# Kernel tuning notes

Measured on AMD Instinct MI355X. Metric: run time of the kernel, lower is better.

## Reference

```python
import jax, jax.numpy as jnp
import numpy as np

B, N, C_IN, C_OUT, K, D_EMB = 32, 4096, 64, 64, 2, 16


def setup_inputs() -> dict:
    key = jax.random.key(0)
    ks = jax.random.split(key, 7)
    x = jax.random.normal(ks[0], (B, N, C_IN), jnp.float32)
    node_embeddings = jax.random.normal(ks[1], (N, D_EMB), jnp.float32)
    weights_pool = jax.random.normal(ks[2], (D_EMB, K, C_IN, C_OUT), jnp.float32) * 0.1
    bias_pool = jax.random.normal(ks[3], (D_EMB, C_OUT), jnp.float32) * 0.1
    lin_w = jax.random.normal(ks[4], (C_OUT, C_IN), jnp.float32) * 0.1
    lin_b = jax.random.normal(ks[5], (C_OUT,), jnp.float32) * 0.1
    adj = jax.random.uniform(ks[6], (N, N), jnp.float32)
    return dict(x=x, node_embeddings=node_embeddings, weights_pool=weights_pool,
                bias_pool=bias_pool, lin_w=lin_w, lin_b=lin_b, adj=adj)


def _sym_norm_adj(W):
    # W + 0.5*I, then D^{-1/2} W D^{-1/2} with D = diag(rowsum)
    n = W.shape[0]
    W = W + 0.5 * jnp.eye(n, dtype=W.dtype)
    sd = jnp.sqrt(1.0 / jnp.sum(W, axis=1))
    return sd[:, None] * W * sd[None, :]


def reference(x, node_embeddings, weights_pool, bias_pool, lin_w, lin_b, adj):
    n = node_embeddings.shape[0]
    # adaptive adjacency: softmax(relu(E E^T)) over neighbors
    supports_dyn = jax.nn.softmax(jax.nn.relu(node_embeddings @ node_embeddings.T), axis=1)
    supports = jnp.stack([jnp.eye(n, dtype=x.dtype), supports_dyn], axis=0)  # [K=2, N, N]
    # node-adaptive weights/bias generated from embeddings
    weights = jnp.einsum('nd,dkio->nkio', node_embeddings, weights_pool)  # [N,K,Cin,Cout]
    bias = node_embeddings @ bias_pool  # [N, Cout]
    # multi-hop aggregation + per-node conv
    x_g = jnp.einsum('knm,bmc->bnkc', supports, x)  # [B,N,K,Cin]
    x_gconv = jnp.einsum('bnki,nkio->bno', x_g, weights) + bias[None]  # [B,N,Cout]
    # static branch: init applies F.softmax(dim=1) to sym-normed adj, forward re-softmaxes dim=-1
    A = jax.nn.softmax(jax.nn.softmax(_sym_norm_adj(adj), axis=1), axis=-1)
    # einsum 'nm,bmc->bmc' == scale node m by sum_n A[n,m]
    scale = jnp.sum(A, axis=0)  # [N]
    x_static = (scale[None, :, None] * x) @ lin_w.T + lin_b  # [B,N,Cout]
    return x_gconv + jax.nn.sigmoid(x_static) * x_static
```

## Files before the change

### kernel.cpp

```cpp
#include <hip/hip_runtime.h>
#include <stdint.h>

#define Bdim 32
#define Ndim 4096
#define Cin  64
#define Cout 64
#define Demb 16

typedef __bf16 bf16x8 __attribute__((ext_vector_type(8)));
typedef float  f32x4  __attribute__((ext_vector_type(4)));

#define GLOBAL_AS(p) ((__attribute__((address_space(1))) void*)(p))
#define LDS_AS(p)    ((__attribute__((address_space(3))) void*)(p))

__device__ __forceinline__ uint16_t f2bf(float x) {
    union { float f; uint32_t u; } v; v.f = x;
    uint32_t r = v.u + 0x7FFFu + ((v.u >> 16) & 1u);
    return (uint16_t)(r >> 16);
}

__device__ __forceinline__ bf16x8 pack8(float4 a, float4 b) {
    union { uint16_t u[8]; bf16x8 v; } r;
    r.u[0] = f2bf(a.x); r.u[1] = f2bf(a.y); r.u[2] = f2bf(a.z); r.u[3] = f2bf(a.w);
    r.u[4] = f2bf(b.x); r.u[5] = f2bf(b.y); r.u[6] = f2bf(b.z); r.u[7] = f2bf(b.w);
    return r.v;
}

__global__ __launch_bounds__(256) void p1_prep(const float* __restrict__ E,
                                               const float* __restrict__ x,
                                               const float* __restrict__ adj,
                                               const float* __restrict__ pool,
                                               uint16_t* __restrict__ A,
                                               float* __restrict__ invA,
                                               uint16_t* __restrict__ Xtt,
                                               float* __restrict__ sd,
                                               float* __restrict__ scale,
                                               float* __restrict__ poolT) {
    __shared__ __align__(16) uint8_t smem[9232];
    const int t = threadIdx.x;
    const int blk = blockIdx.x;

    if (blk < 256) {
        float* Er_s = (float*)smem;
        float* red_s = (float*)(smem + 1024);
        const int n0 = blk * 16;
        Er_s[t] = E[n0 * Demb + t];
        __syncthreads();
        for (int half = 0; half < 2; ++half) {
            float er[8][16];
#pragma unroll
            for (int r = 0; r < 8; ++r)
#pragma unroll
                for (int d = 0; d < 16; ++d) er[r][d] = Er_s[(half * 8 + r) * 16 + d];
            float sacc[8];
#pragma unroll
            for (int r = 0; r < 8; ++r) sacc[r] = 0.f;
            for (int c = 0; c < 16; ++c) {
                const int m = c * 256 + t;
                const float4* ep = (const float4*)(E + (size_t)m * Demb);
                float4 e0 = ep[0], e1 = ep[1], e2 = ep[2], e3 = ep[3];
                float em[16] = {e0.x, e0.y, e0.z, e0.w, e1.x, e1.y, e1.z, e1.w,
                                e2.x, e2.y, e2.z, e2.w, e3.x, e3.y, e3.z, e3.w};
#pragma unroll
                for (int r = 0; r < 8; ++r) {
                    float v = 0.f;
#pragma unroll
                    for (int d = 0; d < 16; ++d) v = fmaf(er[r][d], em[d], v);
                    v = fmaxf(v, 0.f);
                    const float e = __expf(v);
                    sacc[r] += e;
                    A[(size_t)(n0 + half * 8 + r) * Ndim + m] = f2bf(e);
                }
            }
#pragma unroll
            for (int r = 0; r < 8; ++r) {
                float s = sacc[r];
#pragma unroll
                for (int off = 32; off > 0; off >>= 1) s += __shfl_down(s, off, 64);
                __syncthreads();
                if ((t & 63) == 0) red_s[t >> 6] = s;
                __syncthreads();
                if (t == 0)
                    invA[n0 + half * 8 + r] = 1.f / (red_s[0] + red_s[1] + red_s[2] + red_s[3]);
            }
            __syncthreads();
        }
    } else if (blk < 2304) {
        auto T = (uint16_t(*)[72])smem;
        const int idx = blk - 256;
        const int m0 = (idx & 63) * 64;
        const int b = idx >> 6;
        const int c = t & 63;
#pragma unroll
        for (int j = 0; j < 16; ++j) {
            const int m = (t >> 6) + j * 4;
            T[c][m] = f2bf(x[((size_t)b * Ndim + (m0 + m)) * Cin + c]);
        }
        __syncthreads();
        const int c2 = t >> 2, mo = (t & 3) * 16;
        const uint4* src = (const uint4*)&T[c2][mo];
        uint4 v0 = src[0], v1 = src[1];
        uint4* dst = (uint4*)(Xtt + (size_t)(b * Cin + c2) * Ndim + m0 + mo);
        dst[0] = v0;
        dst[1] = v1;
    } else if (blk < 6400) {
        float* red_s = (float*)smem;
        const int n = blk - 2304;
        if (n < 16) scale[n * 256 + t] = 0.f;
        const float4* ap = (const float4*)(adj + (size_t)n * Ndim);
        float s = 0.f;
#pragma unroll
        for (int q = 0; q < 4; ++q) {
            float4 a = ap[q * 256 + t];
            s += a.x + a.y + a.z + a.w;
        }
#pragma unroll
        for (int off = 32; off > 0; off >>= 1) s += __shfl_down(s, off, 64);
        if ((t & 63) == 0) red_s[t >> 6] = s;
        __syncthreads();
        if (t == 0) sd[n] = sqrtf(1.f / (red_s[0] + red_s[1] + red_s[2] + red_s[3] + 0.5f));
    } else {
        const int idx = blk - 6400;
        const int d = idx >> 2;
        const int base = (idx & 3) * 2048;
#pragma unroll
        for (int j = 0; j < 8; ++j) {
            const int e = base + j * 256 + t;
            const float v = pool[d * 8192 + e];
            poolT[d * 8192 + (e & 63) * 128 + (e >> 6)] = v;
        }
    }
}

__global__ __launch_bounds__(256) void p2_mid(const float* __restrict__ E,
                                              const float* __restrict__ adj,
                                              const float* __restrict__ sd,
                                              const float* __restrict__ poolT,
                                              const float* __restrict__ bias_pool,
                                              float* __restrict__ scale,
                                              uint16_t* __restrict__ Wt,
                                              float* __restrict__ biasn) {
    __shared__ __align__(16) uint8_t smem[16384];
    const int t = threadIdx.x;
    const int blk = blockIdx.x;

    if (blk < 256) {
        float* cs = (float*)smem;
#pragma unroll
        for (int i = 0; i < 16; ++i) cs[i * 256 + t] = 0.f;
        __syncthreads();

        const int wv = t >> 6, l = t & 63;
        const int nb = blk * 16 + wv * 4;

        float sdm[64];
#pragma unroll
        for (int i = 0; i < 16; ++i) {
            float4 s4 = *(const float4*)(sd + i * 256 + l * 4);
            sdm[i * 4 + 0] = s4.x; sdm[i * 4 + 1] = s4.y;
            sdm[i * 4 + 2] = s4.z; sdm[i * 4 + 3] = s4.w;
        }
        float colsum[64];
#pragma unroll
        for (int k = 0; k < 64; ++k) colsum[k] = 0.f;

        for (int r = 0; r < 4; ++r) {
            const int n = nb + r;
            const float sdn = sd[n];
            float e1[64];
            float s1 = 0.f;
#pragma unroll
            for (int i = 0; i < 16; ++i) {
                float4 a4 = *(const float4*)(adj + (size_t)n * Ndim + i * 256 + l * 4);
                const int c0 = i * 256 + l * 4;
                float vv[4] = {a4.x, a4.y, a4.z, a4.w};
#pragma unroll
                for (int u = 0; u < 4; ++u) {
                    const float vd = vv[u] + ((c0 + u) == n ? 0.5f : 0.f);
                    const float e = __expf(sdn * vd * sdm[i * 4 + u]);
                    e1[i * 4 + u] = e;
                    s1 += e;
                }
            }
#pragma unroll
            for (int off = 32; off > 0; off >>= 1) s1 += __shfl_xor(s1, off, 64);
            const float inv1 = 1.f / s1;
            float s2 = 0.f;
#pragma unroll
            for (int k = 0; k < 64; ++k) {
                const float e = __expf(e1[k] * inv1);
                e1[k] = e;
                s2 += e;
            }
#pragma unroll
            for (int off = 32; off > 0; off >>= 1) s2 += __shfl_xor(s2, off, 64);
            const float inv2 = 1.f / s2;
#pragma unroll
            for (int k = 0; k < 64; ++k) colsum[k] = fmaf(e1[k], inv2, colsum[k]);
        }
#pragma unroll
        for (int k = 0; k < 64; ++k)
            atomicAdd(&cs[(k >> 2) * 256 + l * 4 + (k & 3)], colsum[k]);
        __syncthreads();
#pragma unroll
        for (int i = 0; i < 16; ++i)
            atomicAdd(scale + i * 256 + t, cs[i * 256 + t]);
    } else {
        float* En = (float*)smem;
        const int idx = blk - 256;
        const int ec = idx & 7;
        const int n0 = (idx >> 3) * 32;
        En[t] = E[n0 * Demb + t];
        En[t + 256] = E[n0 * Demb + t + 256];
        __syncthreads();

        const int e0 = ec * 1024 + t * 4;
        float4 P[16];
#pragma unroll
        for (int d = 0; d < 16; ++d) P[d] = *(const float4*)(poolT + d * 8192 + e0);

        for (int g = 0; g < 32; ++g) {
            float4 acc = {0.f, 0.f, 0.f, 0.f};
#pragma unroll
            for (int d = 0; d < 16; ++d) {
                const float e = En[g * 16 + d];
                acc.x = fmaf(e, P[d].x, acc.x);
                acc.y = fmaf(e, P[d].y, acc.y);
                acc.z = fmaf(e, P[d].z, acc.z);
                acc.w = fmaf(e, P[d].w, acc.w);
            }
            union { uint16_t u[4]; uint2 v; } r;
            r.u[0] = f2bf(acc.x); r.u[1] = f2bf(acc.y);
            r.u[2] = f2bf(acc.z); r.u[3] = f2bf(acc.w);
            *(uint2*)(Wt + (size_t)(n0 + g) * 8192 + e0) = r.v;
        }

        if (ec == 0) {
            const int o = t & 63, gq = t >> 6;
#pragma unroll
            for (int gi = 0; gi < 8; ++gi) {
                const int g = gi * 4 + gq;
                float a = 0.f;
#pragma unroll
                for (int d = 0; d < 16; ++d) a = fmaf(En[g * 16 + d], bias_pool[d * 64 + o], a);
                biasn[(size_t)(n0 + g) * 64 + o] = a;
            }
        }
    }
}

#define GK 4096
#define GN 2048
__global__ __launch_bounds__(256) void k3_gemm(const uint16_t* __restrict__ Abf,
                                               const uint16_t* __restrict__ Bbf,
                                               const float* __restrict__ invA,
                                               uint16_t* __restrict__ Cbf) {
    __shared__ __align__(16) uint16_t As[128 * 32];
    __shared__ __align__(16) uint16_t Bs[128 * 32];
    const int t = threadIdx.x;
    const int lane = t & 63;
    const int w = t >> 6;
    const int wr = w >> 1, wc = w & 1;
    const int bm = blockIdx.y * 128;
    const int bn = blockIdx.x * 128;

    f32x4 acc[4][4];
#pragma unroll
    for (int i = 0; i < 4; ++i)
#pragma unroll
        for (int j = 0; j < 4; ++j) acc[i][j] = (f32x4){0.f, 0.f, 0.f, 0.f};

    const uint16_t* agp[2];
    const uint16_t* bgp[2];
    uint16_t* alp[2];
    uint16_t* blp[2];
#pragma unroll
    for (int i = 0; i < 2; ++i) {
        const int r = w * 32 + i * 16 + (lane >> 2);
        const int cg = (lane & 3) ^ ((r >> 1) & 3);
        agp[i] = Abf + (size_t)(bm + r) * GK + cg * 8;
        bgp[i] = Bbf + (size_t)(bn + r) * GK + cg * 8;
        alp[i] = &As[(w * 32 + i * 16) * 32];
        blp[i] = &Bs[(w * 32 + i * 16) * 32];
    }

    int offA[4], offB[4];
#pragma unroll
    for (int i = 0; i < 4; ++i) {
        const int m = wr * 64 + i * 16 + (lane & 15);
        offA[i] = m * 32 + (((lane >> 4) ^ ((m >> 1) & 3)) * 8);
        const int n = wc * 64 + i * 16 + (lane & 15);
        offB[i] = n * 32 + (((lane >> 4) ^ ((n >> 1) & 3)) * 8);
    }

    for (int kt = 0; kt < GK / 32; ++kt) {
#pragma unroll
        for (int i = 0; i < 2; ++i) {
            __builtin_amdgcn_global_load_lds(GLOBAL_AS(agp[i] + (size_t)kt * 32), LDS_AS(alp[i]), 16, 0, 0);
            __builtin_amdgcn_global_load_lds(GLOBAL_AS(bgp[i] + (size_t)kt * 32), LDS_AS(blp[i]), 16, 0, 0);
        }
        __syncthreads();
        bf16x8 af[4], bfr[4];
#pragma unroll
        for (int i = 0; i < 4; ++i) {
            af[i] = *(const bf16x8*)(As + offA[i]);
            bfr[i] = *(const bf16x8*)(Bs + offB[i]);
        }
#pragma unroll
        for (int i = 0; i < 4; ++i)
#pragma unroll
            for (int j = 0; j < 4; ++j)
                acc[i][j] = __builtin_amdgcn_mfma_f32_16x16x32_bf16(af[i], bfr[j], acc[i][j], 0, 0, 0);
        __syncthreads();
    }
#pragma unroll
    for (int i = 0; i < 4; ++i) {
        float invv[4];
#pragma unroll
        for (int r = 0; r < 4; ++r)
            invv[r] = invA[bm + wr * 64 + i * 16 + (lane >> 4) * 4 + r];
#pragma unroll
        for (int j = 0; j < 4; ++j)
#pragma unroll
            for (int r = 0; r < 4; ++r) {
                const int row = bm + wr * 64 + i * 16 + (lane >> 4) * 4 + r;
                const int col = bn + wc * 64 + j * 16 + (lane & 15);
                Cbf[(size_t)row * GN + col] = f2bf(acc[i][j][r] * invv[r]);
            }
    }
}

__global__ __launch_bounds__(256) void k6_gconv(const float* __restrict__ x,
                                                const uint16_t* __restrict__ XG,
                                                const uint16_t* __restrict__ Wt,
                                                const float* __restrict__ biasn,
                                                const float* __restrict__ scale,
                                                const float* __restrict__ lin_w,
                                                const float* __restrict__ lin_b,
                                                float* __restrict__ out) {
    __shared__ __align__(16) uint16_t Lws[64][72];
    const int t = threadIdx.x;
    const int n0 = blockIdx.x * 4;

    {
        const int o = t >> 2, i0 = (t & 3) * 16;
        const float4* lp = (const float4*)(lin_w + o * 64 + i0);
        float4 a0 = lp[0], a1 = lp[1], a2 = lp[2], a3 = lp[3];
        union { uint16_t u[16]; uint4 v[2]; } r;
        r.u[0] = f2bf(a0.x); r.u[1] = f2bf(a0.y); r.u[2]  = f2bf(a0.z); r.u[3]  = f2bf(a0.w);
        r.u[4] = f2bf(a1.x); r.u[5] = f2bf(a1.y); r.u[6]  = f2bf(a1.z); r.u[7]  = f2bf(a1.w);
        r.u[8] = f2bf(a2.x); r.u[9] = f2bf(a2.y); r.u[10] = f2bf(a2.z); r.u[11] = f2bf(a2.w);
        r.u[12] = f2bf(a3.x); r.u[13] = f2bf(a3.y); r.u[14] = f2bf(a3.z); r.u[15] = f2bf(a3.w);
        *(uint4*)&Lws[o][i0] = r.v[0];
        *(uint4*)&Lws[o][i0 + 8] = r.v[1];
    }

    const int w = t >> 6, lane = t & 63;
    const int n = n0 + w;
    const int l15 = lane & 15;
    const int q8 = (lane >> 4) * 8;

    bf16x8 a[2][4];
#pragma unroll
    for (int mt = 0; mt < 2; ++mt) {
        const int b = mt * 16 + l15;
        const float* xp = x + ((size_t)b * Ndim + n) * 64 + q8;
        a[mt][0] = pack8(((const float4*)xp)[0], ((const float4*)xp)[1]);
        a[mt][1] = pack8(((const float4*)(xp + 32))[0], ((const float4*)(xp + 32))[1]);
        const uint16_t* gp = XG + (size_t)n * 2048 + b * 64 + q8;
        a[mt][2] = *(const bf16x8*)gp;
        a[mt][3] = *(const bf16x8*)(gp + 32);
    }

    f32x4 accg[2][4], accs[2][4];
#pragma unroll
    for (int mt = 0; mt < 2; ++mt)
#pragma unroll
        for (int j = 0; j < 4; ++j) {
            accg[mt][j] = (f32x4){0.f, 0.f, 0.f, 0.f};
            accs[mt][j] = (f32x4){0.f, 0.f, 0.f, 0.f};
        }

    const uint16_t* wp = Wt + (size_t)n * 8192 + l15 * 128 + q8;

    __syncthreads();

#pragma unroll
    for (int ks = 0; ks < 4; ++ks) {
        bf16x8 bw[4];
#pragma unroll
        for (int j = 0; j < 4; ++j)
            bw[j] = *(const bf16x8*)(wp + j * 2048 + ks * 32);
#pragma unroll
        for (int mt = 0; mt < 2; ++mt)
#pragma unroll
            for (int j = 0; j < 4; ++j)
                accg[mt][j] = __builtin_amdgcn_mfma_f32_16x16x32_bf16(a[mt][ks], bw[j], accg[mt][j], 0, 0, 0);
        if (ks < 2) {
            bf16x8 bl[4];
#pragma unroll
            for (int j = 0; j < 4; ++j)
                bl[j] = *(const bf16x8*)&Lws[j * 16 + l15][ks * 32 + q8];
#pragma unroll
            for (int mt = 0; mt < 2; ++mt)
#pragma unroll
                for (int j = 0; j < 4; ++j)
                    accs[mt][j] = __builtin_amdgcn_mfma_f32_16x16x32_bf16(a[mt][ks], bl[j], accs[mt][j], 0, 0, 0);
        }
    }

    const float sc = scale[n];
#pragma unroll
    for (int j = 0; j < 4; ++j) {
        const int o = j * 16 + l15;
        const float bn = biasn[(size_t)n * 64 + o];
        const float lb = lin_b[o];
#pragma unroll
        for (int mt = 0; mt < 2; ++mt)
#pragma unroll
            for (int r = 0; r < 4; ++r) {
                const int b = mt * 16 + (lane >> 4) * 4 + r;
                const float gg = accg[mt][j][r] + bn;
                const float xs = sc * accs[mt][j][r] + lb;
                out[((size_t)b * Ndim + n) * 64 + o] = gg + xs / (1.f + __expf(-xs));
            }
    }
}

extern "C" void kernel_launch(void* const* d_in, const int* in_sizes, int n_in,
                              void* d_out, int out_size, void* d_ws, size_t ws_size,
                              hipStream_t stream) {
    const float* x         = (const float*)d_in[0];
    const float* E         = (const float*)d_in[1];
    const float* pool      = (const float*)d_in[2];
    const float* bias_pool = (const float*)d_in[3];
    const float* lin_w     = (const float*)d_in[4];
    const float* lin_b     = (const float*)d_in[5];
    const float* adj       = (const float*)d_in[6];
    float* out = (float*)d_out;

    uint8_t* ws = (uint8_t*)d_ws;
    uint16_t* A     = (uint16_t*)(ws);
    uint16_t* Xtt   = (uint16_t*)(ws + 33554432);
    uint16_t* XG    = (uint16_t*)(ws + 50331648);
    uint16_t* Wt    = (uint16_t*)(ws + 67108864);
    float*    biasn = (float*)   (ws + 134217728);
    float*    sd    = (float*)   (ws + 135266304);
    float*    scale = (float*)   (ws + 135282688);
    float*    poolT = (float*)   (ws + 135299072);
    float*    invA  = (float*)   (ws + 135823360);

    p1_prep<<<dim3(6464), dim3(256), 0, stream>>>(E, x, adj, pool, A, invA, Xtt, sd, scale, poolT);
    p2_mid<<<dim3(1280), dim3(256), 0, stream>>>(E, adj, sd, poolT, bias_pool, scale, Wt, biasn);
    k3_gemm<<<dim3(16, 32), dim3(256), 0, stream>>>(A, Xtt, invA, XG);
    k6_gconv<<<dim3(1024), dim3(256), 0, stream>>>(x, XG, Wt, biasn, scale, lin_w, lin_b, out);
}
```

Before: 340.4 us.

## Restructure dense GEMM with triple-buffered LDS pipeline and larger 256x128 tiles

The support-by-x GEMM moves from 128x128 tiles with a single LDS buffer and two barriers per 32-wide K step to 256x128 tiles computed by 512 threads. It now uses 64-wide K steps with a three-stage global-to-LDS prefetch, partial vmcnt waits, an XOR swizzle and MFMA priority hints. It also remaps block IDs to group tiles for L2 locality. The aim is to hide global load latency behind MFMA work and cut barrier and load overhead, at the cost of much more LDS use (about 144KB per block) and lower occupancy.

```diff
diff --git a/kernel.cpp b/kernel.cpp
--- a/kernel.cpp
+++ b/kernel.cpp
@@ -12,6 +12,7 @@
 
 #define GLOBAL_AS(p) ((__attribute__((address_space(1))) void*)(p))
 #define LDS_AS(p)    ((__attribute__((address_space(3))) void*)(p))
+#define GLL(gp, lp)  __builtin_amdgcn_global_load_lds(GLOBAL_AS(gp), LDS_AS(lp), 16, 0, 0)
 
 __device__ __forceinline__ uint16_t f2bf(float x) {
     union { float f; uint32_t u; } v; v.f = x;
@@ -251,18 +252,53 @@
 
 #define GK 4096
 #define GN 2048
-__global__ __launch_bounds__(256) void k3_gemm(const uint16_t* __restrict__ Abf,
+#define K3_NT 64
+__global__ __launch_bounds__(512) void k3_gemm(const uint16_t* __restrict__ Abf,
                                                const uint16_t* __restrict__ Bbf,
                                                const float* __restrict__ invA,
                                                uint16_t* __restrict__ Cbf) {
-    __shared__ __align__(16) uint16_t As[128 * 32];
-    __shared__ __align__(16) uint16_t Bs[128 * 32];
+    __shared__ __align__(16) uint16_t As[3][256 * 64];
+    __shared__ __align__(16) uint16_t Bs[3][128 * 64];
     const int t = threadIdx.x;
     const int lane = t & 63;
-    const int w = t >> 6;
-    const int wr = w >> 1, wc = w & 1;
-    const int bm = blockIdx.y * 128;
-    const int bn = blockIdx.x * 128;
+    const int wid = t >> 6;
+    const int wr = wid >> 1;
+    const int wc = wid & 1;
+
+    const int bid = blockIdx.x;
+    const int wgid = (bid & 7) * 32 + (bid >> 3);
+    const int bm = (wgid >> 4) * 256;
+    const int bn = (wgid & 15) * 128;
+
+    const uint16_t* asrc[4];
+    int adst[4];
+#pragma unroll
+    for (int i = 0; i < 4; ++i) {
+        const int c = t + i * 512;
+        const int row = c >> 3, ch = c & 7;
+        asrc[i] = Abf + (size_t)(bm + row) * GK + ((ch ^ (row & 7)) << 3);
+        adst[i] = c << 3;
+    }
+    const uint16_t* bsrc[2];
+    int bdst[2];
+#pragma unroll
+    for (int i = 0; i < 2; ++i) {
+        const int c = t + i * 512;
+        const int row = c >> 3, ch = c & 7;
+        bsrc[i] = Bbf + (size_t)(bn + row) * GK + ((ch ^ (row & 7)) << 3);
+        bdst[i] = c << 3;
+    }
+
+    int offA[4][2], offB[4][2];
+#pragma unroll
+    for (int f = 0; f < 4; ++f)
+#pragma unroll
+        for (int ks = 0; ks < 2; ++ks) {
+            const int ra = wr * 64 + f * 16 + (lane & 15);
+            offA[f][ks] = ra * 64 + (((ks * 4 + (lane >> 4)) ^ (ra & 7)) << 3);
+            const int rb = wc * 64 + f * 16 + (lane & 15);
+            offB[f][ks] = rb * 64 + (((ks * 4 + (lane >> 4)) ^ (rb & 7)) << 3);
+        }
 
     f32x4 acc[4][4];
 #pragma unroll
@@ -270,62 +306,85 @@
 #pragma unroll
         for (int j = 0; j < 4; ++j) acc[i][j] = (f32x4){0.f, 0.f, 0.f, 0.f};
 
-    const uint16_t* agp[2];
-    const uint16_t* bgp[2];
-    uint16_t* alp[2];
-    uint16_t* blp[2];
-#pragma unroll
-    for (int i = 0; i < 2; ++i) {
-        const int r = w * 32 + i * 16 + (lane >> 2);
-        const int cg = (lane & 3) ^ ((r >> 1) & 3);
-        agp[i] = Abf + (size_t)(bm + r) * GK + cg * 8;
-        bgp[i] = Bbf + (size_t)(bn + r) * GK + cg * 8;
-        alp[i] = &As[(w * 32 + i * 16) * 32];
-        blp[i] = &Bs[(w * 32 + i * 16) * 32];
-    }
-
-    int offA[4], offB[4];
-#pragma unroll
-    for (int i = 0; i < 4; ++i) {
-        const int m = wr * 64 + i * 16 + (lane & 15);
-        offA[i] = m * 32 + (((lane >> 4) ^ ((m >> 1) & 3)) * 8);
-        const int n = wc * 64 + i * 16 + (lane & 15);
-        offB[i] = n * 32 + (((lane >> 4) ^ ((n >> 1) & 3)) * 8);
-    }
-
-    for (int kt = 0; kt < GK / 32; ++kt) {
-#pragma unroll
-        for (int i = 0; i < 2; ++i) {
-            __builtin_amdgcn_global_load_lds(GLOBAL_AS(agp[i] + (size_t)kt * 32), LDS_AS(alp[i]), 16, 0, 0);
-            __builtin_amdgcn_global_load_lds(GLOBAL_AS(bgp[i] + (size_t)kt * 32), LDS_AS(blp[i]), 16, 0, 0);
-        }
-        __syncthreads();
-        bf16x8 af[4], bfr[4];
-#pragma unroll
-        for (int i = 0; i < 4; ++i) {
-            af[i] = *(const bf16x8*)(As + offA[i]);
-            bfr[i] = *(const bf16x8*)(Bs + offB[i]);
-        }
-#pragma unroll
-        for (int i = 0; i < 4; ++i)
+#define K3_STAGE(buf, kt)                                  \
+    do {                                                   \
+        const size_t ko_ = (size_t)(kt) * 64;              \
+        GLL(asrc[0] + ko_, &As[buf][adst[0]]);             \
+        GLL(asrc[1] + ko_, &As[buf][adst[1]]);             \
+        GLL(asrc[2] + ko_, &As[buf][adst[2]]);             \
+        GLL(asrc[3] + ko_, &As[buf][adst[3]]);             \
+        GLL(bsrc[0] + ko_, &Bs[buf][bdst[0]]);             \
+        GLL(bsrc[1] + ko_, &Bs[buf][bdst[1]]);             \
+    } while (0)
+
+    K3_STAGE(0, 0);
+    K3_STAGE(1, 1);
+    asm volatile("s_waitcnt vmcnt(6)" ::: "memory");
+    __builtin_amdgcn_s_barrier();
+    asm volatile("" ::: "memory");
+
+    int cur = 0;
+    for (int kt = 0; kt < K3_NT; ++kt) {
+        if (kt < K3_NT - 2) {
+            int nbuf = cur + 2; if (nbuf >= 3) nbuf -= 3;
+            K3_STAGE(nbuf, kt + 2);
+        }
+        const uint16_t* Ab = As[cur];
+        const uint16_t* Bb = Bs[cur];
+
+        bf16x8 a0[4], b0[4];
+#pragma unroll
+        for (int f = 0; f < 4; ++f) a0[f] = *(const bf16x8*)(Ab + offA[f][0]);
+#pragma unroll
+        for (int j = 0; j < 4; ++j) b0[j] = *(const bf16x8*)(Bb + offB[j][0]);
+        __builtin_amdgcn_s_setprio(1);
+#pragma unroll
+        for (int f = 0; f < 4; ++f)
 #pragma unroll
             for (int j = 0; j < 4; ++j)
-                acc[i][j] = __builtin_amdgcn_mfma_f32_16x16x32_bf16(af[i], bfr[j], acc[i][j], 0, 0, 0);
-        __syncthreads();
-    }
-#pragma unroll
-    for (int i = 0; i < 4; ++i) {
+                acc[f][j] = __builtin_amdgcn_mfma_f32_16x16x32_bf16(a0[f], b0[j], acc[f][j], 0, 0, 0);
+        __builtin_amdgcn_s_setprio(0);
+        asm volatile("" ::: "memory");
+        __builtin_amdgcn_s_barrier();
+        asm volatile("" ::: "memory");
+
+        bf16x8 a1[4], b1[4];
+#pragma unroll
+        for (int f = 0; f < 4; ++f) a1[f] = *(const bf16x8*)(Ab + offA[f][1]);
+#pragma unroll
+        for (int j = 0; j < 4; ++j) b1[j] = *(const bf16x8*)(Bb + offB[j][1]);
+        __builtin_amdgcn_s_setprio(1);
+#pragma unroll
+        for (int f = 0; f < 4; ++f)
+#pragma unroll
+            for (int j = 0; j < 4; ++j)
+                acc[f][j] = __builtin_amdgcn_mfma_f32_16x16x32_bf16(a1[f], b1[j], acc[f][j], 0, 0, 0);
+        __builtin_amdgcn_s_setprio(0);
+
+        if (kt < K3_NT - 2)
+            asm volatile("s_waitcnt vmcnt(6)" ::: "memory");
+        else
+            asm volatile("s_waitcnt vmcnt(0)" ::: "memory");
+        __builtin_amdgcn_s_barrier();
+        asm volatile("" ::: "memory");
+
+        if (++cur == 3) cur = 0;
+    }
+#undef K3_STAGE
+
+#pragma unroll
+    for (int f = 0; f < 4; ++f) {
         float invv[4];
 #pragma unroll
         for (int r = 0; r < 4; ++r)
-            invv[r] = invA[bm + wr * 64 + i * 16 + (lane >> 4) * 4 + r];
+            invv[r] = invA[bm + wr * 64 + f * 16 + (lane >> 4) * 4 + r];
 #pragma unroll
         for (int j = 0; j < 4; ++j)
 #pragma unroll
             for (int r = 0; r < 4; ++r) {
-                const int row = bm + wr * 64 + i * 16 + (lane >> 4) * 4 + r;
+                const int row = bm + wr * 64 + f * 16 + (lane >> 4) * 4 + r;
                 const int col = bn + wc * 64 + j * 16 + (lane & 15);
-                Cbf[(size_t)row * GN + col] = f2bf(acc[i][j][r] * invv[r]);
+                Cbf[(size_t)row * GN + col] = f2bf(acc[f][j][r] * invv[r]);
             }
     }
 }
@@ -452,6 +511,6 @@
 
     p1_prep<<<dim3(6464), dim3(256), 0, stream>>>(E, x, adj, pool, A, invA, Xtt, sd, scale, poolT);
     p2_mid<<<dim3(1280), dim3(256), 0, stream>>>(E, adj, sd, poolT, bias_pool, scale, Wt, biasn);
-    k3_gemm<<<dim3(16, 32), dim3(256), 0, stream>>>(A, Xtt, invA, XG);
+    k3_gemm<<<dim3(256), dim3(512), 0, stream>>>(A, Xtt, invA, XG);
     k6_gconv<<<dim3(1024), dim3(256), 0, stream>>>(x, XG, Wt, biasn, scale, lin_w, lin_b, out);
 }
```

After: 351.0 us. 1.03x slower.
